# Kernel tuning notes

Hardware: AMD Instinct MI355X
Metric: run time of the kernel (lower is better)

Reference implementation:

```python
import jax, jax.numpy as jnp
import numpy as np

N, C, H, W = 32, 256, 56, 56
G = 16
EPS = 1e-05
N_ITER = 10


def isqrt_newton_schulz(A, num_iters):
    # A: (G, G) SPD. Returns A^{-1/2} via Newton-Schulz iteration.
    dim = A.shape[0]
    normA = jnp.linalg.norm(A)  # Frobenius norm
    Y = A / normA
    I = jnp.eye(dim, dtype=A.dtype)
    Z = jnp.eye(dim, dtype=A.dtype)
    for _ in range(num_iters):
        T = 0.5 * (3.0 * I - Z @ Y)
        Y = Y @ T
        Z = T @ Z
    return Z / jnp.sqrt(normA)


def setup_inputs() -> dict:
    key = jax.random.key(0)
    k1, = jax.random.split(key, 1)
    x = jax.random.normal(k1, (N, C, H, W), dtype=jnp.float32)
    weight = jnp.ones((1, C, 1, 1), dtype=jnp.float32)
    bias = jnp.zeros((1, C, 1, 1), dtype=jnp.float32)
    return {"x": x, "weight": weight, "bias": bias}


def reference(x, weight, bias):
    n, c_all, h, w = x.shape
    c = (c_all // G) * G  # == c_all here (256 divisible by 16)
    # (N, c/G, G, H, W) -> (G, N, c/G, H, W) -> (G, M)
    x1 = x[:, :c].reshape(n, c // G, G, h, w).transpose(2, 0, 1, 3, 4).reshape(G, -1)
    mean1 = jnp.mean(x1, axis=-1, keepdims=True)  # (G, 1)
    xc = x1 - mean1
    M = xc.shape[1]
    cov = xc @ xc.T / M + EPS * jnp.eye(G, dtype=x.dtype)  # (G, G)
    decorr = isqrt_newton_schulz(cov, N_ITER)  # (G, G)
    y = decorr @ xc  # (G, M) whitening GEMM
    y = y.reshape(G, n, c // G, h, w).transpose(1, 2, 0, 3, 4).reshape(n, c, h, w)
    return y * weight + bias
```

## Files before the change

### kernel.cpp

```cpp
#include <hip/hip_runtime.h>


constexpr int kC    = 256;
constexpr int kHW   = 3136;
constexpr int kP    = 512;
constexpr int kAcc  = 152;
constexpr float kEps = 1e-5f;
constexpr int kNsIter = 10;
constexpr int kSplit = 4;
constexpr int kChunk = 196;

typedef float floatx4 __attribute__((ext_vector_type(4)));

template <int Ctrl, int RowMask>
__device__ __forceinline__ float dpp_fadd(float x) {
  int perm = __builtin_amdgcn_update_dpp(0, __float_as_int(x), Ctrl, RowMask, 0xf, true);
  return x + __int_as_float(perm);
}
__device__ __forceinline__ float wave_sum64(float x) {
  x = dpp_fadd<0xB1, 0xF>(x);
  x = dpp_fadd<0x4E, 0xF>(x);
  x = dpp_fadd<0x124, 0xF>(x);
  x = dpp_fadd<0x128, 0xF>(x);
  x = dpp_fadd<0x142, 0xA>(x);
  x = dpp_fadd<0x143, 0xC>(x);
  return x;
}

__global__ __launch_bounds__(256, 2) void fd_stats(const float* __restrict__ x,
                                                   float* __restrict__ partials) {
  const int p  = blockIdx.x;
  const int n  = p >> 4, c1 = p & 15;
  const float* base = x + (size_t)(n * kC + c1 * 16) * kHW;
  const int t = threadIdx.x;

  float s[16];
  float pr[136];
#pragma unroll
  for (int j = 0; j < 16; ++j) s[j] = 0.f;
#pragma unroll
  for (int a = 0; a < 136; ++a) pr[a] = 0.f;

  for (int ch = t; ch < kHW / 2; ch += 256) {
    float2 v[16];
#pragma unroll
    for (int j = 0; j < 16; ++j)
      v[j] = reinterpret_cast<const float2*>(base + j * kHW)[ch];
#pragma unroll
    for (int j = 0; j < 16; ++j) s[j] += v[j].x + v[j].y;
#pragma unroll
    for (int j = 0; j < 16; ++j) {
#pragma unroll
      for (int k = j; k < 16; ++k) {
        const int idx = j * 16 - (j * (j - 1)) / 2 + (k - j);
        pr[idx] += v[j].x * v[k].x + v[j].y * v[k].y;
      }
    }
  }

  __shared__ float wbuf[4][kAcc];
  const int lane = t & 63, w = t >> 6;
#pragma unroll
  for (int j = 0; j < 16; ++j) {
    float r = wave_sum64(s[j]);
    if (lane == 63) wbuf[w][j] = r;
  }
#pragma unroll
  for (int a = 0; a < 136; ++a) {
    float r = wave_sum64(pr[a]);
    if (lane == 63) wbuf[w][16 + a] = r;
  }
  __syncthreads();
  if (t < kAcc)
    partials[(size_t)p * kAcc + t] =
        (wbuf[0][t] + wbuf[1][t]) + (wbuf[2][t] + wbuf[3][t]);
}

__global__ __launch_bounds__(256) void fd_newton(const float* __restrict__ partials,
                                                 float* __restrict__ params) {
  __shared__ float stats[kAcc];
  __shared__ float meanv[16];
  __shared__ float Yb[2][256];
  __shared__ float Zb[2][256];
  __shared__ float Tm[256];
  __shared__ float redb[4];
  __shared__ float snorm;
  const int t = threadIdx.x;

  if (t < kAcc) {
    const float* q = partials + t;
    float a0=0,a1=0,a2=0,a3=0,a4=0,a5=0,a6=0,a7=0;
    for (int b = 0; b < kP; b += 8) {
      a0 += q[(size_t)(b+0)*kAcc]; a1 += q[(size_t)(b+1)*kAcc];
      a2 += q[(size_t)(b+2)*kAcc]; a3 += q[(size_t)(b+3)*kAcc];
      a4 += q[(size_t)(b+4)*kAcc]; a5 += q[(size_t)(b+5)*kAcc];
      a6 += q[(size_t)(b+6)*kAcc]; a7 += q[(size_t)(b+7)*kAcc];
    }
    stats[t] = ((a0+a1)+(a2+a3)) + ((a4+a5)+(a6+a7));
  }
  __syncthreads();
  constexpr float invM = 1.0f / (float)(kP * kHW);
  if (t < 16) meanv[t] = stats[t] * invM;
  __syncthreads();

  const int i = t >> 4, j = t & 15;
  const int a = i < j ? i : j, b = i < j ? j : i;
  float cij = stats[16 + a * 16 - (a * (a - 1)) / 2 + (b - a)] * invM
              - meanv[i] * meanv[j];
  if (i == j) cij += kEps;

  float r = wave_sum64(cij * cij);
  if ((t & 63) == 63) redb[t >> 6] = r;
  __syncthreads();
  if (t == 0) snorm = sqrtf((redb[0] + redb[1]) + (redb[2] + redb[3]));
  __syncthreads();

  Yb[0][t] = cij * (1.0f / snorm);
  Zb[0][t] = (i == j) ? 1.0f : 0.0f;
  __syncthreads();

  int cur = 0;
  for (int it = 0; it < kNsIter; ++it) {
    float acc = 0.f;
#pragma unroll
    for (int k = 0; k < 16; ++k) acc += Zb[cur][i * 16 + k] * Yb[cur][k * 16 + j];
    Tm[t] = ((i == j) ? 1.5f : 0.0f) - 0.5f * acc;
    __syncthreads();
    float y = 0.f, z = 0.f;
#pragma unroll
    for (int k = 0; k < 16; ++k) {
      y += Yb[cur][i * 16 + k] * Tm[k * 16 + j];
      z += Tm[i * 16 + k] * Zb[cur][k * 16 + j];
    }
    Yb[cur ^ 1][t] = y;
    Zb[cur ^ 1][t] = z;
    cur ^= 1;
    __syncthreads();
  }

  const float D = Zb[cur][t] / sqrtf(snorm);
  params[t] = D;
  Tm[t] = D * meanv[j];
  __syncthreads();
  if (t < 16) {
    float o = 0.f;
#pragma unroll
    for (int k = 0; k < 16; ++k) o += Tm[t * 16 + k];
    params[256 + t] = o;
  }
}

__global__ __launch_bounds__(256, 4) void fd_whiten(const float* __restrict__ x,
                                                    const float* __restrict__ weight,
                                                    const float* __restrict__ bias,
                                                    const float* __restrict__ params,
                                                    float* __restrict__ out) {
  const int blk = blockIdx.x;
  const int p = blk >> 2, s = blk & (kSplit - 1);
  const int n = p >> 4, c1 = p & 15;
  const int t = threadIdx.x;
  const int w    = __builtin_amdgcn_readfirstlane(t >> 6);
  const int lane = t & 63;
  const int g0   = 4 * w;

  const float* base  = x   + (size_t)(n * kC + c1 * 16) * kHW;
  float*       obase = out + (size_t)(n * kC + c1 * 16) * kHW;

  float d[4][16];
#pragma unroll
  for (int gg = 0; gg < 4; ++gg)
#pragma unroll
    for (int j = 0; j < 16; ++j)
      d[gg][j] = params[(g0 + gg) * 16 + j];

  float wv[4], sv[4];
#pragma unroll
  for (int gg = 0; gg < 4; ++gg) {
    const int g  = g0 + gg;
    const int ch = c1 * 16 + g;
    wv[gg] = weight[ch];
    sv[gg] = bias[ch] - params[256 + g] * wv[gg];
  }

  for (int lp = lane; lp < kChunk; lp += 64) {
    const int pos = s * kChunk + lp;
    float4 acc0 = make_float4(0.f, 0.f, 0.f, 0.f);
    float4 acc1 = acc0, acc2 = acc0, acc3 = acc0;
#pragma unroll
    for (int j = 0; j < 16; ++j) {
      const float4 v = reinterpret_cast<const float4*>(base + j * kHW)[pos];
#define ACC(A, dd) A.x += (dd) * v.x; A.y += (dd) * v.y; A.z += (dd) * v.z; A.w += (dd) * v.w;
      ACC(acc0, d[0][j]); ACC(acc1, d[1][j]); ACC(acc2, d[2][j]); ACC(acc3, d[3][j]);
#undef ACC
    }
#define EMIT(A, gg)                                                          \
    {                                                                        \
      floatx4 o;                                                             \
      o.x = A.x * wv[gg] + sv[gg]; o.y = A.y * wv[gg] + sv[gg];              \
      o.z = A.z * wv[gg] + sv[gg]; o.w = A.w * wv[gg] + sv[gg];              \
      __builtin_nontemporal_store(                                           \
          o, reinterpret_cast<floatx4*>(obase + (g0 + gg) * kHW) + pos);     \
    }
    EMIT(acc0, 0) EMIT(acc1, 1) EMIT(acc2, 2) EMIT(acc3, 3)
#undef EMIT
  }
}

extern "C" void kernel_launch(void* const* d_in, const int* in_sizes, int n_in,
                              void* d_out, int out_size, void* d_ws, size_t ws_size,
                              hipStream_t stream) {
  const float* x      = (const float*)d_in[0];
  const float* weight = (const float*)d_in[1];
  const float* bias   = (const float*)d_in[2];
  float* out = (float*)d_out;

  float* wsf      = (float*)d_ws;
  float* partials = wsf;
  float* params   = wsf + (size_t)kP * kAcc;

  fd_stats <<<kP, 256, 0, stream>>>(x, partials);
  fd_newton<<<1,  256, 0, stream>>>(partials, params);
  fd_whiten<<<kP * kSplit, 256, 0, stream>>>(x, weight, bias, params, out);
}
```

Baseline: 94.35 us.

## Split stats kernel across waves via LDS tiles and transposed partials

The stats kernel now stages each block's slice of 16 channels into shared memory. It splits the 136 Gram-matrix entries across the four waves with balanced row sets, so each thread holds 38 accumulators instead of 152. It also launches four times as many blocks, each covering a quarter of the spatial range. Partials are written transposed, so the single-block reduction kernel reads them coalesced with float4 loads and wave reductions. The aim is to cut register pressure and raise occupancy and parallelism in the stats pass, at the cost of an LDS round-trip, extra synchronisation and four times as many partials to reduce.

Result: slower. 105.1 us (+11.4%).

```diff
diff --git a/kernel.cpp b/kernel.cpp
--- a/kernel.cpp
+++ b/kernel.cpp
@@ -9,8 +9,15 @@
 constexpr int kNsIter = 10;
 constexpr int kSplit = 4;
 constexpr int kChunk = 196;
+constexpr int kNB   = kP * 4;
+constexpr int kTileF2 = 196;
+constexpr int kTileF4 = 98;
 
 typedef float floatx4 __attribute__((ext_vector_type(4)));
+
+__device__ __host__ constexpr int triidx(int j, int k) {
+  return j * 16 - (j * (j - 1)) / 2 + (k - j);
+}
 
 template <int Ctrl, int RowMask>
 __device__ __forceinline__ float dpp_fadd(float x) {
@@ -27,56 +34,110 @@
   return x;
 }
 
-__global__ __launch_bounds__(256, 2) void fd_stats(const float* __restrict__ x,
-                                                   float* __restrict__ partials) {
-  const int p  = blockIdx.x;
-  const int n  = p >> 4, c1 = p & 15;
-  const float* base = x + (size_t)(n * kC + c1 * 16) * kHW;
+template <int R0, int R1, int R2, int R3>
+struct RowSet {
+  static constexpr int O0 = 0;
+  static constexpr int O1 = O0 + (16 - R0);
+  static constexpr int O2 = O1 + (16 - R1);
+  static constexpr int O3 = O2 + (16 - R2);
+};
+
+template <int R0, int R1, int R2, int R3, int S0>
+__device__ __forceinline__ void accum_tile(const float2* __restrict__ lds2, int lane,
+                                           float* __restrict__ acc) {
+  using RS = RowSet<R0, R1, R2, R3>;
+  for (int p = lane; p < kTileF2; p += 64) {
+    float2 v[16];
+#pragma unroll
+    for (int c = 0; c < 16; ++c) v[c] = lds2[c * kTileF2 + p];
+#pragma unroll
+    for (int c = 0; c < 4; ++c) acc[34 + c] += v[S0 + c].x + v[S0 + c].y;
+#pragma unroll
+    for (int k = R0; k < 16; ++k) acc[RS::O0 + k - R0] += v[R0].x * v[k].x + v[R0].y * v[k].y;
+#pragma unroll
+    for (int k = R1; k < 16; ++k) acc[RS::O1 + k - R1] += v[R1].x * v[k].x + v[R1].y * v[k].y;
+#pragma unroll
+    for (int k = R2; k < 16; ++k) acc[RS::O2 + k - R2] += v[R2].x * v[k].x + v[R2].y * v[k].y;
+#pragma unroll
+    for (int k = R3; k < 16; ++k) acc[RS::O3 + k - R3] += v[R3].x * v[k].x + v[R3].y * v[k].y;
+  }
+}
+
+template <int R0, int R1, int R2, int R3, int S0>
+__device__ __forceinline__ void write_acc(float* __restrict__ pT, int blk, int lane,
+                                          const float* __restrict__ acc) {
+  using RS = RowSet<R0, R1, R2, R3>;
+#pragma unroll
+  for (int k = R0; k < 16; ++k) {
+    float r = wave_sum64(acc[RS::O0 + k - R0]);
+    if (lane == 63) pT[(size_t)(16 + triidx(R0, k)) * kNB + blk] = r;
+  }
+#pragma unroll
+  for (int k = R1; k < 16; ++k) {
+    float r = wave_sum64(acc[RS::O1 + k - R1]);
+    if (lane == 63) pT[(size_t)(16 + triidx(R1, k)) * kNB + blk] = r;
+  }
+#pragma unroll
+  for (int k = R2; k < 16; ++k) {
+    float r = wave_sum64(acc[RS::O2 + k - R2]);
+    if (lane == 63) pT[(size_t)(16 + triidx(R2, k)) * kNB + blk] = r;
+  }
+#pragma unroll
+  for (int k = R3; k < 16; ++k) {
+    float r = wave_sum64(acc[RS::O3 + k - R3]);
+    if (lane == 63) pT[(size_t)(16 + triidx(R3, k)) * kNB + blk] = r;
+  }
+#pragma unroll
+  for (int c = 0; c < 4; ++c) {
+    float r = wave_sum64(acc[34 + c]);
+    if (lane == 63) pT[(size_t)(S0 + c) * kNB + blk] = r;
+  }
+}
+
+__global__ __launch_bounds__(256, 4) void fd_stats(const float* __restrict__ x,
+                                                   float* __restrict__ pT) {
+  __shared__ __align__(16) float2 tile[16 * kTileF2];
+  const int blk = blockIdx.x;
+  const int p = blk >> 2, s = blk & 3;
+  const int n = p >> 4, c1 = p & 15;
   const int t = threadIdx.x;
-
-  float s[16];
-  float pr[136];
-#pragma unroll
-  for (int j = 0; j < 16; ++j) s[j] = 0.f;
-#pragma unroll
-  for (int a = 0; a < 136; ++a) pr[a] = 0.f;
-
-  for (int ch = t; ch < kHW / 2; ch += 256) {
-    float2 v[16];
-#pragma unroll
-    for (int j = 0; j < 16; ++j)
-      v[j] = reinterpret_cast<const float2*>(base + j * kHW)[ch];
-#pragma unroll
-    for (int j = 0; j < 16; ++j) s[j] += v[j].x + v[j].y;
-#pragma unroll
-    for (int j = 0; j < 16; ++j) {
-#pragma unroll
-      for (int k = j; k < 16; ++k) {
-        const int idx = j * 16 - (j * (j - 1)) / 2 + (k - j);
-        pr[idx] += v[j].x * v[k].x + v[j].y * v[k].y;
-      }
-    }
-  }
-
-  __shared__ float wbuf[4][kAcc];
-  const int lane = t & 63, w = t >> 6;
-#pragma unroll
-  for (int j = 0; j < 16; ++j) {
-    float r = wave_sum64(s[j]);
-    if (lane == 63) wbuf[w][j] = r;
-  }
-#pragma unroll
-  for (int a = 0; a < 136; ++a) {
-    float r = wave_sum64(pr[a]);
-    if (lane == 63) wbuf[w][16 + a] = r;
-  }
-  __syncthreads();
-  if (t < kAcc)
-    partials[(size_t)p * kAcc + t] =
-        (wbuf[0][t] + wbuf[1][t]) + (wbuf[2][t] + wbuf[3][t]);
-}
-
-__global__ __launch_bounds__(256) void fd_newton(const float* __restrict__ partials,
+  const int w = __builtin_amdgcn_readfirstlane(t >> 6);
+  const int lane = t & 63;
+
+  const float4* xb =
+      reinterpret_cast<const float4*>(x) + (size_t)(n * kC + c1 * 16) * (kHW / 4);
+
+  float acc[38];
+#pragma unroll
+  for (int a = 0; a < 38; ++a) acc[a] = 0.f;
+
+  float4* lds4 = reinterpret_cast<float4*>(tile);
+  const float2* lds2 = tile;
+
+  for (int t2 = 0; t2 < 2; ++t2) {
+    if (t2) __syncthreads();
+    const int fbase = s * 196 + t2 * kTileF4;
+    for (int q = t; q < 16 * kTileF4; q += 256) {
+      const int ch = q / kTileF4, fo = q - ch * kTileF4;
+      lds4[ch * kTileF4 + fo] = xb[(size_t)ch * (kHW / 4) + fbase + fo];
+    }
+    __syncthreads();
+    switch (w) {
+      case 0:  accum_tile<0, 1, 14, 15, 0 >(lds2, lane, acc); break;
+      case 1:  accum_tile<2, 3, 12, 13, 4 >(lds2, lane, acc); break;
+      case 2:  accum_tile<4, 5, 10, 11, 8 >(lds2, lane, acc); break;
+      default: accum_tile<6, 7, 8,  9,  12>(lds2, lane, acc); break;
+    }
+  }
+  switch (w) {
+    case 0:  write_acc<0, 1, 14, 15, 0 >(pT, blk, lane, acc); break;
+    case 1:  write_acc<2, 3, 12, 13, 4 >(pT, blk, lane, acc); break;
+    case 2:  write_acc<4, 5, 10, 11, 8 >(pT, blk, lane, acc); break;
+    default: write_acc<6, 7, 8,  9,  12>(pT, blk, lane, acc); break;
+  }
+}
+
+__global__ __launch_bounds__(256) void fd_newton(const float* __restrict__ pT,
                                                  float* __restrict__ params) {
   __shared__ float stats[kAcc];
   __shared__ float meanv[16];
@@ -86,27 +147,28 @@
   __shared__ float redb[4];
   __shared__ float snorm;
   const int t = threadIdx.x;
-
-  if (t < kAcc) {
-    const float* q = partials + t;
-    float a0=0,a1=0,a2=0,a3=0,a4=0,a5=0,a6=0,a7=0;
-    for (int b = 0; b < kP; b += 8) {
-      a0 += q[(size_t)(b+0)*kAcc]; a1 += q[(size_t)(b+1)*kAcc];
-      a2 += q[(size_t)(b+2)*kAcc]; a3 += q[(size_t)(b+3)*kAcc];
-      a4 += q[(size_t)(b+4)*kAcc]; a5 += q[(size_t)(b+5)*kAcc];
-      a6 += q[(size_t)(b+6)*kAcc]; a7 += q[(size_t)(b+7)*kAcc];
-    }
-    stats[t] = ((a0+a1)+(a2+a3)) + ((a4+a5)+(a6+a7));
-  }
-  __syncthreads();
+  const int w = t >> 6, lane = t & 63;
+
+  for (int a = w; a < kAcc; a += 4) {
+    const float4* row = reinterpret_cast<const float4*>(pT + (size_t)a * kNB);
+    float sum = 0.f;
+#pragma unroll
+    for (int i = 0; i < kNB / 4 / 64; ++i) {
+      float4 v = row[i * 64 + lane];
+      sum += (v.x + v.y) + (v.z + v.w);
+    }
+    float r = wave_sum64(sum);
+    if (lane == 63) stats[a] = r;
+  }
+  __syncthreads();
+
   constexpr float invM = 1.0f / (float)(kP * kHW);
   if (t < 16) meanv[t] = stats[t] * invM;
   __syncthreads();
 
   const int i = t >> 4, j = t & 15;
   const int a = i < j ? i : j, b = i < j ? j : i;
-  float cij = stats[16 + a * 16 - (a * (a - 1)) / 2 + (b - a)] * invM
-              - meanv[i] * meanv[j];
+  float cij = stats[16 + triidx(a, b)] * invM - meanv[i] * meanv[j];
   if (i == j) cij += kEps;
 
   float r = wave_sum64(cij * cij);
@@ -216,9 +278,9 @@
 
   float* wsf      = (float*)d_ws;
   float* partials = wsf;
-  float* params   = wsf + (size_t)kP * kAcc;
-
-  fd_stats <<<kP, 256, 0, stream>>>(x, partials);
-  fd_newton<<<1,  256, 0, stream>>>(partials, params);
+  float* params   = wsf + (size_t)kAcc * kNB;
+
+  fd_stats <<<kNB, 256, 0, stream>>>(x, partials);
+  fd_newton<<<1,   256, 0, stream>>>(partials, params);
   fd_whiten<<<kP * kSplit, 256, 0, stream>>>(x, weight, bias, params, out);
 }
```
